# Kernel tuning notes

Hardware: AMD Instinct MI355X
Metric: run time of the kernel (lower is better)

Reference implementation:

```python
import jax, jax.numpy as jnp
import numpy as np

# Sizes (see shape_source)
N_P, N_C, E = 65536, 8192, 131072
D_P, D_C, D_ADD, D_EDGE, D_HID = 80, 48, 16, 8, 64
F_IN = D_P + D_C + D_ADD  # 144, message_input_irreps dim


def setup_inputs() -> dict:
    key = jax.random.key(0)
    ks = jax.random.split(key, 8)
    x_p = jax.random.normal(ks[0], (N_P, D_P), jnp.float32)
    x_c = jax.random.normal(ks[1], (N_C, D_C), jnp.float32)
    src = jax.random.randint(ks[2], (E,), 0, N_C)  # indexes x_c (edge_index[0])
    dst = jax.random.randint(ks[3], (E,), 0, N_P)  # indexes x_p (edge_index[1])
    edge_index = jnp.stack([src, dst], axis=0)
    edge_attr = jax.random.normal(ks[4], (E, D_EDGE), jnp.float32)
    additional_message_features = jax.random.normal(ks[5], (E, D_ADD), jnp.float32)
    batch = jnp.zeros((N_P,), jnp.int32)  # single graph; unused when norm=None
    # Fully-connected tensor-product weights (scalar irreps -> bilinear map) + scalar bias
    W1 = jax.random.normal(ks[6], (F_IN, D_EDGE, D_HID), jnp.float32) / np.float32(np.sqrt(F_IN * D_EDGE))
    b1 = jnp.zeros((D_HID,), jnp.float32)
    W2 = jax.random.normal(ks[7], (D_HID, D_EDGE, D_HID), jnp.float32) / np.float32(np.sqrt(D_HID * D_EDGE))
    b2 = jnp.zeros((D_HID,), jnp.float32)
    return {"x_p": x_p, "x_c": x_c, "edge_index": edge_index, "edge_attr": edge_attr,
            "batch": batch, "additional_message_features": additional_message_features,
            "W1": W1, "b1": b1, "W2": W2, "b2": b2}


def _tp(x, a, W, b):
    """Fully-connected O3 tensor product on scalar irreps: out[e,h] = sum_{f,g} x[e,f] a[e,g] W[f,g,h] + b[h]."""
    # contract feature axis first to avoid the [E, F, G] outer product
    y = (x @ W.reshape(W.shape[0], -1)).reshape(x.shape[0], a.shape[1], -1)  # [E, G, H]
    return jnp.einsum('eg,egh->eh', a, y) + b


def reference(x_p, x_c, edge_index, edge_attr, batch, additional_message_features, W1, b1, W2, b2):
    src, dst = edge_index[0], edge_index[1]
    # gather: [E, D_P + D_C + D_ADD]
    inp = jnp.concatenate([x_p[dst], x_c[src], additional_message_features], axis=-1)
    # two O3TensorProductSwishGate message layers (scalar irreps -> bilinear + swish)
    m = jax.nn.silu(_tp(inp, edge_attr, W1, b1))
    m = jax.nn.silu(_tp(m, edge_attr, W2, b2))
    # scatter-sum over destination (particle) nodes, then concat with residual features
    agg = jax.ops.segment_sum(m, dst, num_segments=x_p.shape[0])
    return jnp.concatenate([x_p, agg], axis=-1)  # [N_P, D_P + D_HID]
```

## Files before the change

### kernel.cpp

```cpp
#include <hip/hip_runtime.h>
#include <hip/hip_bf16.h>

#define E_CNT 131072
#define NP_CNT 65536
#define D_P 80
#define D_C 48
#define D_ADD 16
#define K1 1152
#define K2 512
#define MAXDEG 32

typedef _Float16 f16x8 __attribute__((ext_vector_type(8)));
typedef _Float16 f16x2 __attribute__((ext_vector_type(2)));
typedef float f32x4 __attribute__((ext_vector_type(4)));

union F16x8U { f16x2 h2[4]; f16x8 v8; };

__device__ __forceinline__ float silu_f(float x){
  return x / (1.0f + __expf(-x));
}
__device__ __forceinline__ f16x2 pkrtz(float a, float b){
  return __builtin_bit_cast(f16x2, __builtin_amdgcn_cvt_pkrtz(a, b));
}

__global__ void prep_w_kernel(const float* __restrict__ W1, const float* __restrict__ W2,
                              _Float16* __restrict__ wt1, _Float16* __restrict__ wt2){
  int id = blockIdx.x * 256 + threadIdx.x;
  if (id < 64 * K1){
    int h = id / K1, k = id - h * K1;
    int ks = k >> 5, rem = k & 31, q = rem >> 3, j = rem & 7;
    wt1[id] = (_Float16)W1[(q * 36 + ks) * 512 + j * 64 + h];
  } else {
    int id2 = id - 64 * K1;
    int h = id2 / K2, k = id2 - h * K2;
    int ks = k >> 5, rem = k & 31, q = rem >> 3, j = rem & 7;
    wt2[id2] = (_Float16)W2[(q * 16 + ks) * 512 + j * 64 + h];
  }
}

__global__ void zero_cnt_kernel(int* __restrict__ cnt, int* __restrict__ bsum){
  const int gid = blockIdx.x * 256 + threadIdx.x;
  if (gid < NP_CNT) cnt[gid] = 0;
  else bsum[gid - NP_CNT] = 0;
}
__global__ void fill_slots_kernel(const int* __restrict__ eidx,
                                  int* __restrict__ cnt, int* __restrict__ slots){
  const int e = blockIdx.x * 256 + threadIdx.x;
  const int d = eidx[E_CNT + e];
  const int p = atomicAdd(&cnt[d], 1);
  if (p < MAXDEG) slots[d * MAXDEG + p] = e;
}
__global__ void scanA_kernel(const int* __restrict__ cnt, int* __restrict__ bsum){
  const int t = threadIdx.x;
  int v = min(cnt[blockIdx.x * 256 + t], MAXDEG);
  #pragma unroll
  for (int o = 32; o; o >>= 1) v += __shfl_down(v, o);
  __shared__ int s[4];
  if ((t & 63) == 0) s[t >> 6] = v;
  __syncthreads();
  if (t == 0) bsum[blockIdx.x] = s[0] + s[1] + s[2] + s[3];
}
__global__ void scanB_kernel(const int* __restrict__ bsum, int* __restrict__ boff){
  __shared__ int s[256];
  const int t = threadIdx.x;
  const int v = bsum[t];
  s[t] = v; __syncthreads();
  for (int o = 1; o < 256; o <<= 1){
    int x = (t >= o) ? s[t - o] : 0;
    __syncthreads();
    s[t] += x;
    __syncthreads();
  }
  boff[t] = s[t] - v;
}
__global__ void scanC_emit_kernel(const int* __restrict__ cnt, const int* __restrict__ slots,
                                  const int* __restrict__ boff,
                                  int* __restrict__ off, int* __restrict__ perm){
  __shared__ int s[256];
  const int t = threadIdx.x;
  const int n = blockIdx.x * 256 + t;
  const int v = min(cnt[n], MAXDEG);
  s[t] = v; __syncthreads();
  for (int o = 1; o < 256; o <<= 1){
    int x = (t >= o) ? s[t - o] : 0;
    __syncthreads();
    s[t] += x;
    __syncthreads();
  }
  const int o0 = boff[blockIdx.x] + s[t] - v;
  off[n] = o0;
  for (int j = 0; j < v; ++j) perm[o0 + j] = slots[n * MAXDEG + j];
}

__global__ __launch_bounds__(512, 4) void fused_gemm_kernel(
    const float* __restrict__ x_p, const float* __restrict__ x_c,
    const int* __restrict__ eidx, const float* __restrict__ ea,
    const float* __restrict__ addf, const int* __restrict__ perm,
    const _Float16* __restrict__ wt1, const float* __restrict__ b1,
    const _Float16* __restrict__ wt2, const float* __restrict__ b2,
    _Float16* __restrict__ m2p)
{
  constexpr int CHROW = 136;
  __shared__ _Float16 s_w[2][64 * CHROW];
  __shared__ _Float16 s_m1[256 * 72];

  const int t    = threadIdx.x;
  const int lane = t & 63;
  const int wv   = t >> 6;
  const int wm   = wv >> 1;
  const int wn   = wv & 1;
  const int l15  = lane & 15;
  const int q    = lane >> 4;

  const int EB = blockIdx.x * 256;

  const int idx0 = t * 2, idx1 = t * 2 + 1;
  const int h0 = idx0 >> 4, sl0 = idx0 & 15;
  const int h1 = idx1 >> 4, sl1 = idx1 & 15;
  const int lo0 = h0 * CHROW + sl0 * 8, lo1 = h1 * CHROW + sl1 * 8;
  const size_t g0_1 = (size_t)h0 * K1 + sl0 * 8, g1_1 = (size_t)h1 * K1 + sl1 * 8;
  const size_t g0_2 = (size_t)h0 * K2 + sl0 * 8, g1_2 = (size_t)h1 * K2 + sl1 * 8;

  f16x2 apk[4][4];
  int offP[4], offC[4], offA[4];
  #pragma unroll
  for (int mt = 0; mt < 4; ++mt){
    const int e = perm[EB + wm * 64 + mt * 16 + l15] & (E_CNT - 1);
    const float4* ap = reinterpret_cast<const float4*>(ea + (size_t)e * 8);
    float4 a0 = ap[0], a1 = ap[1];
    apk[mt][0] = pkrtz(a0.x, a0.y);
    apk[mt][1] = pkrtz(a0.z, a0.w);
    apk[mt][2] = pkrtz(a1.x, a1.y);
    apk[mt][3] = pkrtz(a1.z, a1.w);
    const int dn = eidx[E_CNT + e];
    const int sn = eidx[e];
    offP[mt] = dn * D_P;
    offC[mt] = sn * D_C - D_P;
    offA[mt] = e * D_ADD - (D_P + D_C);
  }

  f32x4 acc[4][2];
  #pragma unroll
  for (int mt = 0; mt < 4; ++mt){
    acc[mt][0] = f32x4{0.f,0.f,0.f,0.f};
    acc[mt][1] = f32x4{0.f,0.f,0.f,0.f};
  }

  float4 xc[4], xn[4];
  auto FETCHX = [&](int c, float4* dst){
    const int o = q * 36 + 4 * c;
    #pragma unroll
    for (int mt = 0; mt < 4; ++mt){
      const float* p = (o < D_P) ? (x_p + offP[mt] + o)
                     : (o < D_P + D_C) ? (x_c + offC[mt] + o)
                     : (addf + offA[mt] + o);
      dst[mt] = *reinterpret_cast<const float4*>(p);
    }
  };

  const int wrow = (wn * 32 + l15) * CHROW + q * 8;

  uint4 wr0 = *reinterpret_cast<const uint4*>(wt1 + g0_1);
  uint4 wr1 = *reinterpret_cast<const uint4*>(wt1 + g1_1);
  FETCHX(0, xc);
  *reinterpret_cast<uint4*>(&s_w[0][lo0]) = wr0;
  *reinterpret_cast<uint4*>(&s_w[0][lo1]) = wr1;
  __syncthreads();

  for (int c = 0; c < 9; ++c){
    if (c < 8){
      wr0 = *reinterpret_cast<const uint4*>(wt1 + g0_1 + (c + 1) * 128);
      wr1 = *reinterpret_cast<const uint4*>(wt1 + g1_1 + (c + 1) * 128);
      FETCHX(c + 1, xn);
    }
    const _Float16* buf = s_w[c & 1];
    #pragma unroll
    for (int ksl = 0; ksl < 4; ++ksl){
      f16x8 Bf[2];
      #pragma unroll
      for (int nt = 0; nt < 2; ++nt)
        Bf[nt] = __builtin_bit_cast(f16x8,
            *reinterpret_cast<const uint4*>(&buf[wrow + nt * 16 * CHROW + ksl * 32]));
      #pragma unroll
      for (int mt = 0; mt < 4; ++mt){
        const float xv = (ksl == 0) ? xc[mt].x : (ksl == 1) ? xc[mt].y
                       : (ksl == 2) ? xc[mt].z : xc[mt].w;
        f16x2 xb = pkrtz(xv, xv);
        F16x8U A;
        #pragma unroll
        for (int j = 0; j < 4; ++j) A.h2[j] = xb * apk[mt][j];
        acc[mt][0] = __builtin_amdgcn_mfma_f32_16x16x32_f16(A.v8, Bf[0], acc[mt][0], 0, 0, 0);
        acc[mt][1] = __builtin_amdgcn_mfma_f32_16x16x32_f16(A.v8, Bf[1], acc[mt][1], 0, 0, 0);
      }
    }
    if (c < 8){
      _Float16* nb = s_w[(c + 1) & 1];
      *reinterpret_cast<uint4*>(&nb[lo0]) = wr0;
      *reinterpret_cast<uint4*>(&nb[lo1]) = wr1;
      #pragma unroll
      for (int mt = 0; mt < 4; ++mt) xc[mt] = xn[mt];
    }
    __syncthreads();
  }

  wr0 = *reinterpret_cast<const uint4*>(wt2 + g0_2);
  wr1 = *reinterpret_cast<const uint4*>(wt2 + g1_2);

  {
    float bv[2];
    bv[0] = b1[wn * 32 + l15];
    bv[1] = b1[wn * 32 + 16 + l15];
    #pragma unroll
    for (int mt = 0; mt < 4; ++mt){
      #pragma unroll
      for (int nt = 0; nt < 2; ++nt){
        #pragma unroll
        for (int r = 0; r < 4; ++r){
          float s = silu_f(acc[mt][nt][r] + bv[nt]);
          const int eo = wm * 64 + mt * 16 + q * 4 + r;
          const int h  = wn * 32 + nt * 16 + l15;
          s_m1[eo * 72 + h] = (_Float16)s;
        }
      }
    }
  }
  __syncthreads();

  uint4 md[4][2];
  #pragma unroll
  for (int mt = 0; mt < 4; ++mt){
    const int eo = wm * 64 + mt * 16 + l15;
    const uint4* mp = reinterpret_cast<const uint4*>(&s_m1[eo * 72 + q * 16]);
    md[mt][0] = mp[0];
    md[mt][1] = mp[1];
  }
  *reinterpret_cast<uint4*>(&s_w[0][lo0]) = wr0;
  *reinterpret_cast<uint4*>(&s_w[0][lo1]) = wr1;
  #pragma unroll
  for (int mt = 0; mt < 4; ++mt){
    acc[mt][0] = f32x4{0.f,0.f,0.f,0.f};
    acc[mt][1] = f32x4{0.f,0.f,0.f,0.f};
  }
  __syncthreads();

  for (int c = 0; c < 4; ++c){
    if (c < 3){
      wr0 = *reinterpret_cast<const uint4*>(wt2 + g0_2 + (c + 1) * 128);
      wr1 = *reinterpret_cast<const uint4*>(wt2 + g1_2 + (c + 1) * 128);
    }
    const _Float16* buf = s_w[c & 1];
    #pragma unroll
    for (int ksl = 0; ksl < 4; ++ksl){
      f16x8 Bf[2];
      #pragma unroll
      for (int nt = 0; nt < 2; ++nt)
        Bf[nt] = __builtin_bit_cast(f16x8,
            *reinterpret_cast<const uint4*>(&buf[wrow + nt * 16 * CHROW + ksl * 32]));
      const int ks = c * 4 + ksl;
      #pragma unroll
      for (int mt = 0; mt < 4; ++mt){
        const unsigned comp = (ks < 8)
            ? ((ks >> 1) == 0 ? md[mt][0].x : (ks >> 1) == 1 ? md[mt][0].y
             : (ks >> 1) == 2 ? md[mt][0].z : md[mt][0].w)
            : (((ks - 8) >> 1) == 0 ? md[mt][1].x : ((ks - 8) >> 1) == 1 ? md[mt][1].y
             : ((ks - 8) >> 1) == 2 ? md[mt][1].z : md[mt][1].w);
        const unsigned v = (ks & 1) ? (comp >> 16) : (comp & 0xffffu);
        f16x2 xb = __builtin_bit_cast(f16x2, v | (v << 16));
        F16x8U A;
        #pragma unroll
        for (int j = 0; j < 4; ++j) A.h2[j] = xb * apk[mt][j];
        acc[mt][0] = __builtin_amdgcn_mfma_f32_16x16x32_f16(A.v8, Bf[0], acc[mt][0], 0, 0, 0);
        acc[mt][1] = __builtin_amdgcn_mfma_f32_16x16x32_f16(A.v8, Bf[1], acc[mt][1], 0, 0, 0);
      }
    }
    if (c < 3){
      _Float16* nb = s_w[(c + 1) & 1];
      *reinterpret_cast<uint4*>(&nb[lo0]) = wr0;
      *reinterpret_cast<uint4*>(&nb[lo1]) = wr1;
    }
    __syncthreads();
  }

  {
    float bv[2];
    bv[0] = b2[wn * 32 + l15];
    bv[1] = b2[wn * 32 + 16 + l15];
    #pragma unroll
    for (int mt = 0; mt < 4; ++mt){
      #pragma unroll
      for (int nt = 0; nt < 2; ++nt){
        #pragma unroll
        for (int r = 0; r < 4; ++r){
          float s = silu_f(acc[mt][nt][r] + bv[nt]);
          const int eo = wm * 64 + mt * 16 + q * 4 + r;
          const int h  = wn * 32 + nt * 16 + l15;
          m2p[(size_t)(EB + eo) * 64 + h] = (_Float16)s;
        }
      }
    }
  }
}

__global__ __launch_bounds__(256) void combine_kernel(
    const float* __restrict__ x_p, const int* __restrict__ cnt,
    const int* __restrict__ off, const _Float16* __restrict__ m2p,
    float* __restrict__ out)
{
  const int gid = blockIdx.x * 256 + threadIdx.x;
  const int n = gid >> 3;
  const int r = gid & 7;
  const float* ps = x_p + (size_t)n * D_P;
  float* po = out + (size_t)n * 144;
  #pragma unroll
  for (int i = 0; i < 3; ++i){
    const int j4 = r + 8 * i;
    if (j4 < 20)
      *reinterpret_cast<float4*>(po + 4 * j4) = *reinterpret_cast<const float4*>(ps + 4 * j4);
  }
  float s[8] = {0.f,0.f,0.f,0.f,0.f,0.f,0.f,0.f};
  const int o0 = off[n];
  const int d  = min(cnt[n], MAXDEG);
  for (int j = 0; j < d; ++j){
    const uint4 mv = *reinterpret_cast<const uint4*>(m2p + (size_t)(o0 + j) * 64 + r * 8);
    f16x8 mh = __builtin_bit_cast(f16x8, mv);
    #pragma unroll
    for (int k = 0; k < 8; ++k) s[k] += (float)mh[k];
  }
  float4 o0v = make_float4(s[0], s[1], s[2], s[3]);
  float4 o1v = make_float4(s[4], s[5], s[6], s[7]);
  *reinterpret_cast<float4*>(po + 80 + r * 8)     = o0v;
  *reinterpret_cast<float4*>(po + 80 + r * 8 + 4) = o1v;
}

extern "C" void kernel_launch(void* const* d_in, const int* in_sizes, int n_in,
                              void* d_out, int out_size, void* d_ws, size_t ws_size,
                              hipStream_t stream){
  const float* x_p  = (const float*)d_in[0];
  const float* x_c  = (const float*)d_in[1];
  const int*   eidx = (const int*)d_in[2];
  const float* ea   = (const float*)d_in[3];
  const float* addf = (const float*)d_in[5];
  const float* W1   = (const float*)d_in[6];
  const float* b1   = (const float*)d_in[7];
  const float* W2   = (const float*)d_in[8];
  const float* b2   = (const float*)d_in[9];
  float* out = (float*)d_out;

  char* ws = (char*)d_ws;
  _Float16* wt1 = (_Float16*)(ws);
  _Float16* wt2 = (_Float16*)(ws + 163840);
  int* cnt   = (int*)(ws + 262144);
  int* bsum  = (int*)(ws + 524288);
  int* boff  = (int*)(ws + 525312);
  int* off   = (int*)(ws + 526336);
  int* slots = (int*)(ws + 788480);
  int* perm  = (int*)(ws + 9177088);
  _Float16* m2p = (_Float16*)(ws + 9701376);

  prep_w_kernel<<<(64 * K1 + 64 * K2) / 256, 256, 0, stream>>>(W1, W2, wt1, wt2);
  zero_cnt_kernel<<<(NP_CNT + 256) / 256, 256, 0, stream>>>(cnt, bsum);
  fill_slots_kernel<<<E_CNT / 256, 256, 0, stream>>>(eidx, cnt, slots);
  scanA_kernel<<<NP_CNT / 256, 256, 0, stream>>>(cnt, bsum);
  scanB_kernel<<<1, 256, 0, stream>>>(bsum, boff);
  scanC_emit_kernel<<<NP_CNT / 256, 256, 0, stream>>>(cnt, slots, boff, off, perm);
  fused_gemm_kernel<<<E_CNT / 256, 512, 0, stream>>>(
      x_p, x_c, eidx, ea, addf, perm, wt1, b1, wt2, b2, m2p);
  combine_kernel<<<NP_CNT * 8 / 256, 256, 0, stream>>>(x_p, cnt, off, m2p, out);
}
```

Measured before the change: 92.84 us.

## Load weight fragments directly from global in MFMA layout, drop LDS staging

Reorders the preprocessed fp16 weights so that each MFMA B fragment is a contiguous 16-byte vector read straight from global memory, and removes the double-buffered LDS weight tiles and their per-chunk barriers in both GEMM stages. The gathered activation loads switch to a three-deep register prefetch ring and the loops are fully unrolled. This is meant to cut LDS traffic, shared memory use and synchronisation, relying on L1/L2 to serve the small weight set that every wave rereads. The cost is more global or cache load traffic, and the larger unrolled register footprint may limit occupancy.

After: 102.0 us. 9.9% more time.

```diff
diff --git a/kernel.cpp b/kernel.cpp
--- a/kernel.cpp
+++ b/kernel.cpp
@@ -24,17 +24,17 @@
 }
 
 __global__ void prep_w_kernel(const float* __restrict__ W1, const float* __restrict__ W2,
-                              _Float16* __restrict__ wt1, _Float16* __restrict__ wt2){
+                              _Float16* __restrict__ wtf1, _Float16* __restrict__ wtf2){
   int id = blockIdx.x * 256 + threadIdx.x;
   if (id < 64 * K1){
-    int h = id / K1, k = id - h * K1;
-    int ks = k >> 5, rem = k & 31, q = rem >> 3, j = rem & 7;
-    wt1[id] = (_Float16)W1[(q * 36 + ks) * 512 + j * 64 + h];
+    int ks = id >> 11, rem = id & 2047, h = rem >> 5, kk = rem & 31;
+    int q = kk >> 3, j = kk & 7;
+    wtf1[id] = (_Float16)W1[(q * 36 + ks) * 512 + j * 64 + h];
   } else {
     int id2 = id - 64 * K1;
-    int h = id2 / K2, k = id2 - h * K2;
-    int ks = k >> 5, rem = k & 31, q = rem >> 3, j = rem & 7;
-    wt2[id2] = (_Float16)W2[(q * 16 + ks) * 512 + j * 64 + h];
+    int ks = id2 >> 11, rem = id2 & 2047, h = rem >> 5, kk = rem & 31;
+    int q = kk >> 3, j = kk & 7;
+    wtf2[id2] = (_Float16)W2[(q * 16 + ks) * 512 + j * 64 + h];
   }
 }
 
@@ -96,12 +96,10 @@
     const float* __restrict__ x_p, const float* __restrict__ x_c,
     const int* __restrict__ eidx, const float* __restrict__ ea,
     const float* __restrict__ addf, const int* __restrict__ perm,
-    const _Float16* __restrict__ wt1, const float* __restrict__ b1,
-    const _Float16* __restrict__ wt2, const float* __restrict__ b2,
+    const _Float16* __restrict__ wtf1, const float* __restrict__ b1,
+    const _Float16* __restrict__ wtf2, const float* __restrict__ b2,
     _Float16* __restrict__ m2p)
 {
-  constexpr int CHROW = 136;
-  __shared__ _Float16 s_w[2][64 * CHROW];
   __shared__ _Float16 s_m1[256 * 72];
 
   const int t    = threadIdx.x;
@@ -114,12 +112,7 @@
 
   const int EB = blockIdx.x * 256;
 
-  const int idx0 = t * 2, idx1 = t * 2 + 1;
-  const int h0 = idx0 >> 4, sl0 = idx0 & 15;
-  const int h1 = idx1 >> 4, sl1 = idx1 & 15;
-  const int lo0 = h0 * CHROW + sl0 * 8, lo1 = h1 * CHROW + sl1 * 8;
-  const size_t g0_1 = (size_t)h0 * K1 + sl0 * 8, g1_1 = (size_t)h1 * K1 + sl1 * 8;
-  const size_t g0_2 = (size_t)h0 * K2 + sl0 * 8, g1_2 = (size_t)h1 * K2 + sl1 * 8;
+  const int wb = (wn * 32 + l15) * 32 + q * 8;
 
   f16x2 apk[4][4];
   int offP[4], offC[4], offA[4];
@@ -146,7 +139,7 @@
     acc[mt][1] = f32x4{0.f,0.f,0.f,0.f};
   }
 
-  float4 xc[4], xn[4];
+  float4 xb[3][4];
   auto FETCHX = [&](int c, float4* dst){
     const int o = q * 36 + 4 * c;
     #pragma unroll
@@ -158,53 +151,34 @@
     }
   };
 
-  const int wrow = (wn * 32 + l15) * CHROW + q * 8;
-
-  uint4 wr0 = *reinterpret_cast<const uint4*>(wt1 + g0_1);
-  uint4 wr1 = *reinterpret_cast<const uint4*>(wt1 + g1_1);
-  FETCHX(0, xc);
-  *reinterpret_cast<uint4*>(&s_w[0][lo0]) = wr0;
-  *reinterpret_cast<uint4*>(&s_w[0][lo1]) = wr1;
-  __syncthreads();
-
+  FETCHX(0, xb[0]); FETCHX(1, xb[1]); FETCHX(2, xb[2]);
+  #pragma unroll
   for (int c = 0; c < 9; ++c){
-    if (c < 8){
-      wr0 = *reinterpret_cast<const uint4*>(wt1 + g0_1 + (c + 1) * 128);
-      wr1 = *reinterpret_cast<const uint4*>(wt1 + g1_1 + (c + 1) * 128);
-      FETCHX(c + 1, xn);
-    }
-    const _Float16* buf = s_w[c & 1];
+    float4 cur[4];
+    #pragma unroll
+    for (int mt = 0; mt < 4; ++mt) cur[mt] = xb[c % 3][mt];
+    if (c + 3 < 9) FETCHX(c + 3, xb[c % 3]);
     #pragma unroll
     for (int ksl = 0; ksl < 4; ++ksl){
+      const int ks = c * 4 + ksl;
       f16x8 Bf[2];
       #pragma unroll
       for (int nt = 0; nt < 2; ++nt)
         Bf[nt] = __builtin_bit_cast(f16x8,
-            *reinterpret_cast<const uint4*>(&buf[wrow + nt * 16 * CHROW + ksl * 32]));
+            *reinterpret_cast<const uint4*>(wtf1 + ks * 2048 + nt * 512 + wb));
       #pragma unroll
       for (int mt = 0; mt < 4; ++mt){
-        const float xv = (ksl == 0) ? xc[mt].x : (ksl == 1) ? xc[mt].y
-                       : (ksl == 2) ? xc[mt].z : xc[mt].w;
-        f16x2 xb = pkrtz(xv, xv);
+        const float xv = (ksl == 0) ? cur[mt].x : (ksl == 1) ? cur[mt].y
+                       : (ksl == 2) ? cur[mt].z : cur[mt].w;
+        f16x2 xh = pkrtz(xv, xv);
         F16x8U A;
         #pragma unroll
-        for (int j = 0; j < 4; ++j) A.h2[j] = xb * apk[mt][j];
+        for (int j = 0; j < 4; ++j) A.h2[j] = xh * apk[mt][j];
         acc[mt][0] = __builtin_amdgcn_mfma_f32_16x16x32_f16(A.v8, Bf[0], acc[mt][0], 0, 0, 0);
         acc[mt][1] = __builtin_amdgcn_mfma_f32_16x16x32_f16(A.v8, Bf[1], acc[mt][1], 0, 0, 0);
       }
     }
-    if (c < 8){
-      _Float16* nb = s_w[(c + 1) & 1];
-      *reinterpret_cast<uint4*>(&nb[lo0]) = wr0;
-      *reinterpret_cast<uint4*>(&nb[lo1]) = wr1;
-      #pragma unroll
-      for (int mt = 0; mt < 4; ++mt) xc[mt] = xn[mt];
-    }
-    __syncthreads();
-  }
-
-  wr0 = *reinterpret_cast<const uint4*>(wt2 + g0_2);
-  wr1 = *reinterpret_cast<const uint4*>(wt2 + g1_2);
+  }
 
   {
     float bv[2];
@@ -233,52 +207,32 @@
     const uint4* mp = reinterpret_cast<const uint4*>(&s_m1[eo * 72 + q * 16]);
     md[mt][0] = mp[0];
     md[mt][1] = mp[1];
-  }
-  *reinterpret_cast<uint4*>(&s_w[0][lo0]) = wr0;
-  *reinterpret_cast<uint4*>(&s_w[0][lo1]) = wr1;
-  #pragma unroll
-  for (int mt = 0; mt < 4; ++mt){
     acc[mt][0] = f32x4{0.f,0.f,0.f,0.f};
     acc[mt][1] = f32x4{0.f,0.f,0.f,0.f};
   }
-  __syncthreads();
-
-  for (int c = 0; c < 4; ++c){
-    if (c < 3){
-      wr0 = *reinterpret_cast<const uint4*>(wt2 + g0_2 + (c + 1) * 128);
-      wr1 = *reinterpret_cast<const uint4*>(wt2 + g1_2 + (c + 1) * 128);
-    }
-    const _Float16* buf = s_w[c & 1];
-    #pragma unroll
-    for (int ksl = 0; ksl < 4; ++ksl){
-      f16x8 Bf[2];
-      #pragma unroll
-      for (int nt = 0; nt < 2; ++nt)
-        Bf[nt] = __builtin_bit_cast(f16x8,
-            *reinterpret_cast<const uint4*>(&buf[wrow + nt * 16 * CHROW + ksl * 32]));
-      const int ks = c * 4 + ksl;
-      #pragma unroll
-      for (int mt = 0; mt < 4; ++mt){
-        const unsigned comp = (ks < 8)
-            ? ((ks >> 1) == 0 ? md[mt][0].x : (ks >> 1) == 1 ? md[mt][0].y
-             : (ks >> 1) == 2 ? md[mt][0].z : md[mt][0].w)
-            : (((ks - 8) >> 1) == 0 ? md[mt][1].x : ((ks - 8) >> 1) == 1 ? md[mt][1].y
-             : ((ks - 8) >> 1) == 2 ? md[mt][1].z : md[mt][1].w);
-        const unsigned v = (ks & 1) ? (comp >> 16) : (comp & 0xffffu);
-        f16x2 xb = __builtin_bit_cast(f16x2, v | (v << 16));
-        F16x8U A;
-        #pragma unroll
-        for (int j = 0; j < 4; ++j) A.h2[j] = xb * apk[mt][j];
-        acc[mt][0] = __builtin_amdgcn_mfma_f32_16x16x32_f16(A.v8, Bf[0], acc[mt][0], 0, 0, 0);
-        acc[mt][1] = __builtin_amdgcn_mfma_f32_16x16x32_f16(A.v8, Bf[1], acc[mt][1], 0, 0, 0);
-      }
-    }
-    if (c < 3){
-      _Float16* nb = s_w[(c + 1) & 1];
-      *reinterpret_cast<uint4*>(&nb[lo0]) = wr0;
-      *reinterpret_cast<uint4*>(&nb[lo1]) = wr1;
-    }
-    __syncthreads();
+
+  #pragma unroll
+  for (int ks = 0; ks < 16; ++ks){
+    f16x8 Bf[2];
+    #pragma unroll
+    for (int nt = 0; nt < 2; ++nt)
+      Bf[nt] = __builtin_bit_cast(f16x8,
+          *reinterpret_cast<const uint4*>(wtf2 + ks * 2048 + nt * 512 + wb));
+    #pragma unroll
+    for (int mt = 0; mt < 4; ++mt){
+      const unsigned comp = (ks < 8)
+          ? ((ks >> 1) == 0 ? md[mt][0].x : (ks >> 1) == 1 ? md[mt][0].y
+           : (ks >> 1) == 2 ? md[mt][0].z : md[mt][0].w)
+          : (((ks - 8) >> 1) == 0 ? md[mt][1].x : ((ks - 8) >> 1) == 1 ? md[mt][1].y
+           : ((ks - 8) >> 1) == 2 ? md[mt][1].z : md[mt][1].w);
+      const unsigned v = (ks & 1) ? (comp >> 16) : (comp & 0xffffu);
+      f16x2 xh = __builtin_bit_cast(f16x2, v | (v << 16));
+      F16x8U A;
+      #pragma unroll
+      for (int j = 0; j < 4; ++j) A.h2[j] = xh * apk[mt][j];
+      acc[mt][0] = __builtin_amdgcn_mfma_f32_16x16x32_f16(A.v8, Bf[0], acc[mt][0], 0, 0, 0);
+      acc[mt][1] = __builtin_amdgcn_mfma_f32_16x16x32_f16(A.v8, Bf[1], acc[mt][1], 0, 0, 0);
+    }
   }
 
   {
@@ -347,8 +301,8 @@
   float* out = (float*)d_out;
 
   char* ws = (char*)d_ws;
-  _Float16* wt1 = (_Float16*)(ws);
-  _Float16* wt2 = (_Float16*)(ws + 163840);
+  _Float16* wtf1 = (_Float16*)(ws);
+  _Float16* wtf2 = (_Float16*)(ws + 163840);
   int* cnt   = (int*)(ws + 262144);
   int* bsum  = (int*)(ws + 524288);
   int* boff  = (int*)(ws + 525312);
@@ -357,13 +311,13 @@
   int* perm  = (int*)(ws + 9177088);
   _Float16* m2p = (_Float16*)(ws + 9701376);
 
-  prep_w_kernel<<<(64 * K1 + 64 * K2) / 256, 256, 0, stream>>>(W1, W2, wt1, wt2);
+  prep_w_kernel<<<(64 * K1 + 64 * K2) / 256, 256, 0, stream>>>(W1, W2, wtf1, wtf2);
   zero_cnt_kernel<<<(NP_CNT + 256) / 256, 256, 0, stream>>>(cnt, bsum);
   fill_slots_kernel<<<E_CNT / 256, 256, 0, stream>>>(eidx, cnt, slots);
   scanA_kernel<<<NP_CNT / 256, 256, 0, stream>>>(cnt, bsum);
   scanB_kernel<<<1, 256, 0, stream>>>(bsum, boff);
   scanC_emit_kernel<<<NP_CNT / 256, 256, 0, stream>>>(cnt, slots, boff, off, perm);
   fused_gemm_kernel<<<E_CNT / 256, 512, 0, stream>>>(
-      x_p, x_c, eidx, ea, addf, perm, wt1, b1, wt2, b2, m2p);
+      x_p, x_c, eidx, ea, addf, perm, wtf1, b1, wtf2, b2, m2p);
   combine_kernel<<<NP_CNT * 8 / 256, 256, 0, stream>>>(x_p, cnt, off, m2p, out);
 }
```

## Pre-gather edge inputs into packed fp16 rows before fused GEMM

Applied to the files above, without the earlier changes.

Adds a separate kernel that gathers x_p, x_c, additional features and edge attributes per permuted edge into a contiguous fp16 row buffer (152 halves per edge). The fused GEMM kernel then reads contiguous fp16 rows instead of doing scattered fp32 gathers with index indirection inside the MFMA loop. This is meant to cut gather latency and register/address pressure in the main kernel, at the cost of an extra launch and an extra write+read of about 40 MB of intermediate data.

Result: slower. 106.5 us (+14.7%).

```diff
diff --git a/kernel.cpp b/kernel.cpp
--- a/kernel.cpp
+++ b/kernel.cpp
@@ -9,18 +9,23 @@
 #define K1 1152
 #define K2 512
 #define MAXDEG 32
+#define XROW 152
 
 typedef _Float16 f16x8 __attribute__((ext_vector_type(8)));
 typedef _Float16 f16x2 __attribute__((ext_vector_type(2)));
 typedef float f32x4 __attribute__((ext_vector_type(4)));
 
 union F16x8U { f16x2 h2[4]; f16x8 v8; };
+union U4F2  { uint4 u; f16x2 h2[4]; };
 
 __device__ __forceinline__ float silu_f(float x){
   return x / (1.0f + __expf(-x));
 }
 __device__ __forceinline__ f16x2 pkrtz(float a, float b){
   return __builtin_bit_cast(f16x2, __builtin_amdgcn_cvt_pkrtz(a, b));
+}
+__device__ __forceinline__ unsigned pkrtz_u(float a, float b){
+  return __builtin_bit_cast(unsigned, __builtin_amdgcn_cvt_pkrtz(a, b));
 }
 
 __global__ void prep_w_kernel(const float* __restrict__ W1, const float* __restrict__ W2,
@@ -92,10 +97,42 @@
   for (int j = 0; j < v; ++j) perm[o0 + j] = slots[n * MAXDEG + j];
 }
 
+__global__ __launch_bounds__(256) void gather_perm_kernel(
+    const float* __restrict__ x_p, const float* __restrict__ x_c,
+    const float* __restrict__ addf, const float* __restrict__ ea,
+    const int* __restrict__ eidx, const int* __restrict__ perm,
+    _Float16* __restrict__ xgp)
+{
+  const int gid = blockIdx.x * 256 + threadIdx.x;
+  const int pos = gid >> 3;
+  const int r = gid & 7;
+  const int e = perm[pos] & (E_CNT - 1);
+  const int dst = eidx[E_CNT + e];
+  const int src = eidx[e];
+  const float* pP = x_p  + (size_t)dst * D_P;
+  const float* pC = x_c  + (size_t)src * D_C;
+  const float* pA = addf + (size_t)e   * D_ADD;
+  const float* pE = ea   + (size_t)e   * 8;
+  _Float16* orow = xgp + (size_t)pos * XROW;
+  #pragma unroll
+  for (int i = 0; i < 5; ++i){
+    const int jq = r + 8 * i;
+    if (jq < 38){
+      const float* p = (jq < 20) ? (pP + 4 * jq)
+                     : (jq < 32) ? (pC + 4 * (jq - 20))
+                     : (jq < 36) ? (pA + 4 * (jq - 32))
+                     : (pE + 4 * (jq - 36));
+      float4 v = *reinterpret_cast<const float4*>(p);
+      uint2 o;
+      o.x = pkrtz_u(v.x, v.y);
+      o.y = pkrtz_u(v.z, v.w);
+      *reinterpret_cast<uint2*>(orow + 4 * jq) = o;
+    }
+  }
+}
+
 __global__ __launch_bounds__(512, 4) void fused_gemm_kernel(
-    const float* __restrict__ x_p, const float* __restrict__ x_c,
-    const int* __restrict__ eidx, const float* __restrict__ ea,
-    const float* __restrict__ addf, const int* __restrict__ perm,
+    const _Float16* __restrict__ xgp,
     const _Float16* __restrict__ wt1, const float* __restrict__ b1,
     const _Float16* __restrict__ wt2, const float* __restrict__ b2,
     _Float16* __restrict__ m2p)
@@ -122,21 +159,17 @@
   const size_t g0_2 = (size_t)h0 * K2 + sl0 * 8, g1_2 = (size_t)h1 * K2 + sl1 * 8;
 
   f16x2 apk[4][4];
-  int offP[4], offC[4], offA[4];
+  size_t xbase[4];
   #pragma unroll
   for (int mt = 0; mt < 4; ++mt){
-    const int e = perm[EB + wm * 64 + mt * 16 + l15] & (E_CNT - 1);
-    const float4* ap = reinterpret_cast<const float4*>(ea + (size_t)e * 8);
-    float4 a0 = ap[0], a1 = ap[1];
-    apk[mt][0] = pkrtz(a0.x, a0.y);
-    apk[mt][1] = pkrtz(a0.z, a0.w);
-    apk[mt][2] = pkrtz(a1.x, a1.y);
-    apk[mt][3] = pkrtz(a1.z, a1.w);
-    const int dn = eidx[E_CNT + e];
-    const int sn = eidx[e];
-    offP[mt] = dn * D_P;
-    offC[mt] = sn * D_C - D_P;
-    offA[mt] = e * D_ADD - (D_P + D_C);
+    const size_t pos = EB + wm * 64 + mt * 16 + l15;
+    U4F2 af;
+    af.u = *reinterpret_cast<const uint4*>(xgp + pos * XROW + 144);
+    apk[mt][0] = af.h2[0];
+    apk[mt][1] = af.h2[1];
+    apk[mt][2] = af.h2[2];
+    apk[mt][3] = af.h2[3];
+    xbase[mt] = pos * XROW + q * 36;
   }
 
   f32x4 acc[4][2];
@@ -146,16 +179,11 @@
     acc[mt][1] = f32x4{0.f,0.f,0.f,0.f};
   }
 
-  float4 xc[4], xn[4];
-  auto FETCHX = [&](int c, float4* dst){
-    const int o = q * 36 + 4 * c;
-    #pragma unroll
-    for (int mt = 0; mt < 4; ++mt){
-      const float* p = (o < D_P) ? (x_p + offP[mt] + o)
-                     : (o < D_P + D_C) ? (x_c + offC[mt] + o)
-                     : (addf + offA[mt] + o);
-      dst[mt] = *reinterpret_cast<const float4*>(p);
-    }
+  uint2 xc[4], xn[4];
+  auto FETCHX = [&](int c, uint2* dstv){
+    #pragma unroll
+    for (int mt = 0; mt < 4; ++mt)
+      dstv[mt] = *reinterpret_cast<const uint2*>(xgp + xbase[mt] + 4 * c);
   };
 
   const int wrow = (wn * 32 + l15) * CHROW + q * 8;
@@ -183,12 +211,12 @@
             *reinterpret_cast<const uint4*>(&buf[wrow + nt * 16 * CHROW + ksl * 32]));
       #pragma unroll
       for (int mt = 0; mt < 4; ++mt){
-        const float xv = (ksl == 0) ? xc[mt].x : (ksl == 1) ? xc[mt].y
-                       : (ksl == 2) ? xc[mt].z : xc[mt].w;
-        f16x2 xb = pkrtz(xv, xv);
+        const unsigned comp = (ksl < 2) ? xc[mt].x : xc[mt].y;
+        const unsigned v = (ksl & 1) ? (comp >> 16) : (comp & 0xffffu);
+        f16x2 xh = __builtin_bit_cast(f16x2, v | (v << 16));
         F16x8U A;
         #pragma unroll
-        for (int j = 0; j < 4; ++j) A.h2[j] = xb * apk[mt][j];
+        for (int j = 0; j < 4; ++j) A.h2[j] = xh * apk[mt][j];
         acc[mt][0] = __builtin_amdgcn_mfma_f32_16x16x32_f16(A.v8, Bf[0], acc[mt][0], 0, 0, 0);
         acc[mt][1] = __builtin_amdgcn_mfma_f32_16x16x32_f16(A.v8, Bf[1], acc[mt][1], 0, 0, 0);
       }
@@ -233,14 +261,11 @@
     const uint4* mp = reinterpret_cast<const uint4*>(&s_m1[eo * 72 + q * 16]);
     md[mt][0] = mp[0];
     md[mt][1] = mp[1];
+    acc[mt][0] = f32x4{0.f,0.f,0.f,0.f};
+    acc[mt][1] = f32x4{0.f,0.f,0.f,0.f};
   }
   *reinterpret_cast<uint4*>(&s_w[0][lo0]) = wr0;
   *reinterpret_cast<uint4*>(&s_w[0][lo1]) = wr1;
-  #pragma unroll
-  for (int mt = 0; mt < 4; ++mt){
-    acc[mt][0] = f32x4{0.f,0.f,0.f,0.f};
-    acc[mt][1] = f32x4{0.f,0.f,0.f,0.f};
-  }
   __syncthreads();
 
   for (int c = 0; c < 4; ++c){
@@ -265,10 +290,10 @@
             : (((ks - 8) >> 1) == 0 ? md[mt][1].x : ((ks - 8) >> 1) == 1 ? md[mt][1].y
              : ((ks - 8) >> 1) == 2 ? md[mt][1].z : md[mt][1].w);
         const unsigned v = (ks & 1) ? (comp >> 16) : (comp & 0xffffu);
-        f16x2 xb = __builtin_bit_cast(f16x2, v | (v << 16));
+        f16x2 xh = __builtin_bit_cast(f16x2, v | (v << 16));
         F16x8U A;
         #pragma unroll
-        for (int j = 0; j < 4; ++j) A.h2[j] = xb * apk[mt][j];
+        for (int j = 0; j < 4; ++j) A.h2[j] = xh * apk[mt][j];
         acc[mt][0] = __builtin_amdgcn_mfma_f32_16x16x32_f16(A.v8, Bf[0], acc[mt][0], 0, 0, 0);
         acc[mt][1] = __builtin_amdgcn_mfma_f32_16x16x32_f16(A.v8, Bf[1], acc[mt][1], 0, 0, 0);
       }
@@ -356,6 +381,7 @@
   int* slots = (int*)(ws + 788480);
   int* perm  = (int*)(ws + 9177088);
   _Float16* m2p = (_Float16*)(ws + 9701376);
+  _Float16* xgp = (_Float16*)(ws + 26478592);
 
   prep_w_kernel<<<(64 * K1 + 64 * K2) / 256, 256, 0, stream>>>(W1, W2, wt1, wt2);
   zero_cnt_kernel<<<(NP_CNT + 256) / 256, 256, 0, stream>>>(cnt, bsum);
@@ -363,7 +389,7 @@
   scanA_kernel<<<NP_CNT / 256, 256, 0, stream>>>(cnt, bsum);
   scanB_kernel<<<1, 256, 0, stream>>>(bsum, boff);
   scanC_emit_kernel<<<NP_CNT / 256, 256, 0, stream>>>(cnt, slots, boff, off, perm);
-  fused_gemm_kernel<<<E_CNT / 256, 512, 0, stream>>>(
-      x_p, x_c, eidx, ea, addf, perm, wt1, b1, wt2, b2, m2p);
+  gather_perm_kernel<<<E_CNT * 8 / 256, 256, 0, stream>>>(x_p, x_c, addf, ea, eidx, perm, xgp);
+  fused_gemm_kernel<<<E_CNT / 256, 512, 0, stream>>>(xgp, wt1, b1, wt2, b2, m2p);
   combine_kernel<<<NP_CNT * 8 / 256, 256, 0, stream>>>(x_p, cnt, off, m2p, out);
 }
```
